# Performance work log

Hardware: AMD Instinct MI355X
Metric: run time of the kernel (lower is better)

Reference implementation:

```python
import jax, jax.numpy as jnp
import numpy as np

B, T, C, H = 4, 2048, 768, 12
D = C // H  # head dim = 64


def setup_inputs() -> dict:
    key = jax.random.key(0)
    ks = jax.random.split(key, 4)
    scale = 0.02
    return {
        "x": jax.random.normal(ks[0], (B, T, C), dtype=jnp.float32),
        "W_attn": jax.random.normal(ks[1], (C, 3 * C), dtype=jnp.float32) * scale,
        "b_attn": jnp.zeros((3 * C,), dtype=jnp.float32),
        "W_proj": jax.random.normal(ks[2], (C, C), dtype=jnp.float32) * scale,
        "b_proj": jnp.zeros((C,), dtype=jnp.float32),
    }


def reference(x, W_attn, b_attn, W_proj, b_proj):
    Bsz, Tlen, Cdim = x.shape
    qkv = x @ W_attn + b_attn                    # [B,T,3C]
    q, k, v = jnp.split(qkv, 3, axis=-1)          # each [B,T,C]
    # [B,T,C] -> [B,H,T,D]
    def heads(t):
        return t.reshape(Bsz, Tlen, H, D).transpose(0, 2, 1, 3)
    q, k, v = heads(q), heads(k), heads(v)
    att = jnp.einsum("bhqd,bhkd->bhqk", q, k) * (1.0 / np.sqrt(D))
    # causal mask: position q attends to k <= q
    mask = jnp.tril(jnp.ones((Tlen, Tlen), dtype=bool))
    att = jnp.where(mask[None, None], att, -jnp.inf)
    att = jax.nn.softmax(att, axis=-1)
    y = jnp.einsum("bhqk,bhkd->bhqd", att, v)     # [B,H,T,D]
    y = y.transpose(0, 2, 1, 3).reshape(Bsz, Tlen, Cdim)
    return y @ W_proj + b_proj
```

## Files before the change

kernel.cpp:

```cpp
#include <hip/hip_runtime.h>

#define B_SZ   4
#define T_LEN  2048
#define C_DIM  768
#define H_NUM  12
#define THREEC (3 * C_DIM)
#define M_ROWS (B_SZ * T_LEN)
#define CAST_N8 (M_ROWS * C_DIM / 8)
#define CAST_BLOCKS (CAST_N8 / 256)
#define TP_BX ((THREEC + C_DIM) / 32)
#define TP_BY (C_DIM / 32)

typedef _Float16 f16;
typedef _Float16 half8 __attribute__((ext_vector_type(8)));
typedef _Float16 half4 __attribute__((ext_vector_type(4)));
typedef __fp16   pk2   __attribute__((ext_vector_type(2)));
typedef float    f32x4 __attribute__((ext_vector_type(4)));

#define GLD16(gaddr, laddr)                                                         \
  __builtin_amdgcn_global_load_lds(                                                 \
      (const __attribute__((address_space(1))) unsigned int*)(gaddr),               \
      (__attribute__((address_space(3))) unsigned int*)(laddr), 16, 0, 0)
#define MFMA16(a, b, c) __builtin_amdgcn_mfma_f32_16x16x32_f16(a, b, c, 0, 0, 0)

__global__ __launch_bounds__(256) void prep_kernel(
    const float* __restrict__ x, f16* __restrict__ xh,
    const float* __restrict__ Wa, const float* __restrict__ Wp,
    f16* __restrict__ WtA, f16* __restrict__ WtP) {
  __shared__ f16 tile[32][33];
  const int bid = blockIdx.x;
  if (bid < CAST_BLOCKS) {
    int i = bid * 256 + threadIdx.x;
    const float* s = x + (size_t)i * 8;
    half8 h;
#pragma unroll
    for (int u = 0; u < 8; ++u) h[u] = (f16)s[u];
    *(half8*)(xh + (size_t)i * 8) = h;
    return;
  }
  const int t = bid - CAST_BLOCKS;
  int bx = t % TP_BX;
  const int by = t / TP_BX;
  const float* W; f16* Wt; int N;
  if (bx < THREEC / 32) { W = Wa; Wt = WtA; N = THREEC; }
  else { W = Wp; Wt = WtP; N = C_DIM; bx -= THREEC / 32; }
  const int n0 = bx * 32, k0 = by * 32;
  const int tx = threadIdx.x & 31, ty = threadIdx.x >> 5;
#pragma unroll
  for (int i = 0; i < 4; ++i)
    tile[ty + i * 8][tx] = (f16)W[(size_t)(k0 + ty + i * 8) * N + n0 + tx];
  __syncthreads();
#pragma unroll
  for (int i = 0; i < 4; ++i)
    Wt[(size_t)(n0 + ty + i * 8) * C_DIM + k0 + tx] = tile[tx][ty + i * 8];
}

template <int BM, int BN, int OUT_F16, int SWZ>
__global__ __launch_bounds__(256) void gemm_f16_kernel(
    const f16* __restrict__ A, const f16* __restrict__ Bt,
    const float* __restrict__ bias, f16* __restrict__ OutH,
    float* __restrict__ OutF, int M, int N, int K) {
  __shared__ f16 As[BM * 64];
  __shared__ f16 Bs[BN * 64];
  const int tid = threadIdx.x;
  const int lane = tid & 63, wave = tid >> 6;
  const int lm = lane & 15, kq = lane >> 4, lm7 = lm & 7;
  constexpr int MT = BM / 32, NT = BN / 32;
  const int wm = (wave & 1) * (BM / 2), wn = (wave >> 1) * (BN / 2);

  int bx = blockIdx.x, by = blockIdx.y;
  if (SWZ) {
    const int nx = gridDim.x;
    const int lin = by * nx + bx;
    const int cpx = (nx * gridDim.y) >> 3;
    const int swz = (lin & 7) * cpx + (lin >> 3);
    bx = swz % nx;
    by = swz / nx;
  }
  const int row0 = by * BM, col0 = bx * BN;

  f32x4 acc[MT][NT] = {};

  for (int k0 = 0; k0 < K; k0 += 64) {
    __syncthreads();
#pragma unroll
    for (int i = 0; i < BM / 32; ++i) {
      int c = tid + i * 256;
      int r = c >> 3, cc = (c & 7) ^ (r & 7);
      GLD16(&A[(size_t)(row0 + r) * K + k0 + cc * 8],
            &As[(i * 256 + wave * 64) * 8]);
    }
#pragma unroll
    for (int i = 0; i < BN / 32; ++i) {
      int c = tid + i * 256;
      int r = c >> 3, cc = (c & 7) ^ (r & 7);
      GLD16(&Bt[(size_t)(col0 + r) * K + k0 + cc * 8],
            &Bs[(i * 256 + wave * 64) * 8]);
    }
    __syncthreads();
#pragma unroll
    for (int ks = 0; ks < 2; ++ks) {
      const int pos = (ks * 4 + kq);
      half8 af[MT], bf[NT];
#pragma unroll
      for (int t = 0; t < MT; ++t)
        af[t] = *(const half8*)&As[(wm + t * 16 + lm) * 64 + (pos ^ lm7) * 8];
#pragma unroll
      for (int t = 0; t < NT; ++t)
        bf[t] = *(const half8*)&Bs[(wn + t * 16 + lm) * 64 + (pos ^ lm7) * 8];
#pragma unroll
      for (int mt = 0; mt < MT; ++mt)
#pragma unroll
        for (int nt = 0; nt < NT; ++nt)
          acc[mt][nt] = MFMA16(af[mt], bf[nt], acc[mt][nt]);
    }
  }

#pragma unroll
  for (int mt = 0; mt < MT; ++mt) {
    const int row = row0 + wm + mt * 16 + kq * 4;
#pragma unroll
    for (int nt = 0; nt < NT; ++nt) {
      const int col = col0 + wn + nt * 16 + lm;
      const float bv = bias[col];
#pragma unroll
      for (int r = 0; r < 4; ++r) {
        float v = acc[mt][nt][r] + bv;
        if (OUT_F16)
          OutH[(size_t)(row + r) * N + col] = (f16)v;
        else
          OutF[(size_t)(row + r) * N + col] = v;
      }
    }
  }
}

__global__ __launch_bounds__(256) void v_transpose_kernel(
    const f16* __restrict__ qkv, f16* __restrict__ vt) {
  __shared__ f16 tile[64 * 68];
  const int bh = blockIdx.x, b = bh / H_NUM, h = bh % H_NUM;
  const int t0 = blockIdx.y * 64;
  const int tid = threadIdx.x;
#pragma unroll
  for (int i = 0; i < 2; ++i) {
    int c = tid + i * 256;
    int tr = c >> 3, doff = (c & 7) * 8;
    int pcol = ((tr >> 5) << 5) | (((tr >> 2) & 3) << 3) |
               (((tr >> 4) & 1) << 2) | (tr & 3);
    half8 v = *(const half8*)&qkv[(size_t)(b * T_LEN + t0 + tr) * THREEC + 2 * C_DIM + h * 64 + doff];
#pragma unroll
    for (int u = 0; u < 8; ++u) tile[(doff + u) * 68 + pcol] = v[u];
  }
  __syncthreads();
#pragma unroll
  for (int i = 0; i < 2; ++i) {
    int c = tid + i * 256;
    int d = c >> 3, toff = (c & 7) * 8;
    half8 v;
#pragma unroll
    for (int u = 0; u < 8; ++u) v[u] = tile[d * 68 + toff + u];
    *(half8*)&vt[((size_t)bh * 64 + d) * T_LEN + t0 + toff] = v;
  }
}

__global__ __launch_bounds__(256, 3) void attn_kernel(
    const f16* __restrict__ qkv, const f16* __restrict__ vt,
    f16* __restrict__ y) {
  __shared__ f16 Kt[2][64 * 64];
  __shared__ f16 Vt[2][64 * 64];

  const int bh = blockIdx.x, b = bh / H_NUM, h = bh % H_NUM;
  const int yb = blockIdx.y;
  const int qb = 15 - yb;
  const int tid = threadIdx.x, lane = tid & 63, wave = tid >> 6;
  const int lm = lane & 15, kq = lane >> 4, lm7 = lm & 7;
  const int cw = qb * 2 + (wave >> 1);
  const int qw = qb * 128 + wave * 32;
  const f16 qscale = (f16)(0.125f * 1.44269504f);

  half8 vones;
#pragma unroll
  for (int u = 0; u < 8; ++u) vones[u] = (f16)1.f;

  half8 bq[2][2];
#pragma unroll
  for (int cq = 0; cq < 2; ++cq)
#pragma unroll
    for (int c2 = 0; c2 < 2; ++c2) {
      half8 v = *(const half8*)&qkv[(size_t)(b * T_LEN + qw + cq * 16 + lm) * THREEC +
                                    h * 64 + c2 * 32 + kq * 8];
      bq[cq][c2] = v * qscale;
    }

  f32x4 o[4][2] = {};
  f32x4 ol[2] = {};

  f32x4 fz = {};
  asm volatile("" : "+v"(fz));

  const int srow = tid >> 3;
  const int scol = ((tid & 7) ^ (srow & 7)) * 8;
  const f16* kp = &qkv[(size_t)(b * T_LEN + srow) * THREEC + C_DIM + h * 64 + scol];
  const f16* vp = &vt[((size_t)bh * 64 + srow) * T_LEN + scol];
  const size_t kp2 = (size_t)32 * THREEC;
  const size_t vp2 = (size_t)32 * T_LEN;

  const int sbase = wave * 512;

  const int n_tiles = qb * 2 + 2;

  GLD16(kp, &Kt[0][sbase]);
  GLD16(kp + kp2, &Kt[0][2048 + sbase]);
  GLD16(vp, &Vt[0][sbase]);
  GLD16(vp + vp2, &Vt[0][2048 + sbase]);
  kp += (size_t)64 * THREEC;
  vp += 64;

  for (int it = 0; it < n_tiles; ++it) {
    const int cur = it & 1;
    if (it + 1 < n_tiles) {
      GLD16(kp, &Kt[cur ^ 1][sbase]);
      GLD16(kp + kp2, &Kt[cur ^ 1][2048 + sbase]);
      GLD16(vp, &Vt[cur ^ 1][sbase]);
      GLD16(vp + vp2, &Vt[cur ^ 1][2048 + sbase]);
      kp += (size_t)64 * THREEC;
      vp += 64;
      asm volatile("s_waitcnt vmcnt(4)" ::: "memory");
    } else {
      asm volatile("s_waitcnt vmcnt(0)" ::: "memory");
    }
    __builtin_amdgcn_s_barrier();

    if (it <= cw) {
      f32x4 s4[4][2];
#pragma unroll
      for (int ct = 0; ct < 4; ++ct) {
        const f16* kr = &Kt[cur][(ct * 16 + lm) * 64];
        half8 ak0 = *(const half8*)&kr[(kq ^ lm7) * 8];
        half8 ak1 = *(const half8*)&kr[((4 + kq) ^ lm7) * 8];
#pragma unroll
        for (int cq = 0; cq < 2; ++cq) {
          f32x4 z = MFMA16(ak0, bq[cq][0], fz);
          s4[ct][cq] = MFMA16(ak1, bq[cq][1], z);
        }
      }
      if (it == cw) {
        const int j0 = it * 64;
#pragma unroll
        for (int ct = 0; ct < 4; ++ct)
#pragma unroll
          for (int cq = 0; cq < 2; ++cq) {
            const int qrow = qw + cq * 16 + lm;
#pragma unroll
            for (int r = 0; r < 4; ++r)
              if (j0 + ct * 16 + kq * 4 + r > qrow) s4[ct][cq][r] = -1e30f;
          }
      }
      union { half8 h8; pk2 p2[4]; } pa0[2], pa1[2];
#pragma unroll
      for (int cq = 0; cq < 2; ++cq) {
        pa0[cq].p2[0] = __builtin_amdgcn_cvt_pkrtz(
            __builtin_amdgcn_exp2f(s4[0][cq][0]), __builtin_amdgcn_exp2f(s4[0][cq][1]));
        pa0[cq].p2[1] = __builtin_amdgcn_cvt_pkrtz(
            __builtin_amdgcn_exp2f(s4[0][cq][2]), __builtin_amdgcn_exp2f(s4[0][cq][3]));
        pa0[cq].p2[2] = __builtin_amdgcn_cvt_pkrtz(
            __builtin_amdgcn_exp2f(s4[1][cq][0]), __builtin_amdgcn_exp2f(s4[1][cq][1]));
        pa0[cq].p2[3] = __builtin_amdgcn_cvt_pkrtz(
            __builtin_amdgcn_exp2f(s4[1][cq][2]), __builtin_amdgcn_exp2f(s4[1][cq][3]));
        pa1[cq].p2[0] = __builtin_amdgcn_cvt_pkrtz(
            __builtin_amdgcn_exp2f(s4[2][cq][0]), __builtin_amdgcn_exp2f(s4[2][cq][1]));
        pa1[cq].p2[1] = __builtin_amdgcn_cvt_pkrtz(
            __builtin_amdgcn_exp2f(s4[2][cq][2]), __builtin_amdgcn_exp2f(s4[2][cq][3]));
        pa1[cq].p2[2] = __builtin_amdgcn_cvt_pkrtz(
            __builtin_amdgcn_exp2f(s4[3][cq][0]), __builtin_amdgcn_exp2f(s4[3][cq][1]));
        pa1[cq].p2[3] = __builtin_amdgcn_cvt_pkrtz(
            __builtin_amdgcn_exp2f(s4[3][cq][2]), __builtin_amdgcn_exp2f(s4[3][cq][3]));
      }

#pragma unroll
      for (int dt = 0; dt < 4; ++dt) {
        const f16* vr = &Vt[cur][(dt * 16 + lm) * 64];
        half8 bv0 = *(const half8*)&vr[(kq ^ lm7) * 8];
        half8 bv1 = *(const half8*)&vr[((4 + kq) ^ lm7) * 8];
#pragma unroll
        for (int cq = 0; cq < 2; ++cq) {
          o[dt][cq] = MFMA16(pa0[cq].h8, bv0, o[dt][cq]);
          o[dt][cq] = MFMA16(pa1[cq].h8, bv1, o[dt][cq]);
        }
      }
#pragma unroll
      for (int cq = 0; cq < 2; ++cq) {
        ol[cq] = MFMA16(pa0[cq].h8, vones, ol[cq]);
        ol[cq] = MFMA16(pa1[cq].h8, vones, ol[cq]);
      }
    }

    __builtin_amdgcn_s_barrier();
  }

#pragma unroll
  for (int cq = 0; cq < 2; ++cq)
#pragma unroll
    for (int r = 0; r < 4; ++r) {
      const float inv = 1.f / ol[cq][r];
      const size_t base =
          (size_t)(b * T_LEN + qw + cq * 16 + kq * 4 + r) * C_DIM + h * 64;
#pragma unroll
      for (int dt = 0; dt < 4; ++dt)
        y[base + dt * 16 + lm] = (f16)(o[dt][cq][r] * inv);
    }
}

extern "C" void kernel_launch(void* const* d_in, const int* in_sizes, int n_in,
                              void* d_out, int out_size, void* d_ws, size_t ws_size,
                              hipStream_t stream) {
  const float* x      = (const float*)d_in[0];
  const float* W_attn = (const float*)d_in[1];
  const float* b_attn = (const float*)d_in[2];
  const float* W_proj = (const float*)d_in[3];
  const float* b_proj = (const float*)d_in[4];
  float* out = (float*)d_out;

  const int M = M_ROWS;
  auto align256 = [](size_t v) { return (v + 255) & ~(size_t)255; };
  char* ws = (char*)d_ws;
  f16* xh   = (f16*)ws; ws += align256((size_t)M * C_DIM * 2);
  f16* WtA  = (f16*)ws; ws += align256((size_t)THREEC * C_DIM * 2);
  f16* WtP  = (f16*)ws; ws += align256((size_t)C_DIM * C_DIM * 2);
  f16* qkvh = (f16*)ws; ws += align256((size_t)M * THREEC * 2);
  f16* vtg  = (f16*)ws; ws += align256((size_t)B_SZ * H_NUM * 64 * T_LEN * 2);
  f16* yh   = (f16*)ws; ws += align256((size_t)M * C_DIM * 2);

  prep_kernel<<<CAST_BLOCKS + TP_BX * TP_BY, 256, 0, stream>>>(
      x, xh, W_attn, W_proj, WtA, WtP);

  gemm_f16_kernel<128, 128, 1, 1><<<dim3(THREEC / 128, M / 128), 256, 0, stream>>>(
      xh, WtA, b_attn, qkvh, nullptr, M, THREEC, C_DIM);

  v_transpose_kernel<<<dim3(B_SZ * H_NUM, T_LEN / 64), 256, 0, stream>>>(qkvh, vtg);

  attn_kernel<<<dim3(B_SZ * H_NUM, 16), 256, 0, stream>>>(qkvh, vtg, yh);

  gemm_f16_kernel<128, 64, 0, 1><<<dim3(C_DIM / 64, M / 128), 256, 0, stream>>>(
      yh, WtP, b_proj, nullptr, out, M, C_DIM, C_DIM);
}
```

Measured before the change: 187.7 us.

## Double-buffer GEMM LDS tiles with K=32 stages and async prefetch

Replaces the single-buffered K=64 LDS tile loop in the f16 GEMM with a two-stage double buffer of K=32 tiles. The next tile is prefetched with global_load_lds while MFMAs run on the current one, using explicit vmcnt waits and raw s_barrier instead of __syncthreads. The XOR swizzle is adapted to 4 chunks per row. This is meant to hide global-load latency, at the cost of halving K work per barrier, adding a second barrier per iteration, and relying on hand-counted vmcnt values that must match the number of issued loads.

```diff
diff --git a/kernel.cpp b/kernel.cpp
--- a/kernel.cpp
+++ b/kernel.cpp
@@ -60,11 +60,13 @@
     const f16* __restrict__ A, const f16* __restrict__ Bt,
     const float* __restrict__ bias, f16* __restrict__ OutH,
     float* __restrict__ OutF, int M, int N, int K) {
-  __shared__ f16 As[BM * 64];
-  __shared__ f16 Bs[BN * 64];
+  __shared__ f16 As[2][BM * 32];
+  __shared__ f16 Bs[2][BN * 32];
   const int tid = threadIdx.x;
   const int lane = tid & 63, wave = tid >> 6;
-  const int lm = lane & 15, kq = lane >> 4, lm7 = lm & 7;
+  const int lm = lane & 15, kq = lane >> 4;
+  const int lmx = (lm >> 1) & 3;
+  const int rchunk = (kq ^ lmx) * 8;
   constexpr int MT = BM / 32, NT = BN / 32;
   const int wm = (wave & 1) * (BM / 2), wn = (wave >> 1) * (BN / 2);
 
@@ -81,39 +83,53 @@
 
   f32x4 acc[MT][NT] = {};
 
-  for (int k0 = 0; k0 < K; k0 += 64) {
-    __syncthreads();
-#pragma unroll
-    for (int i = 0; i < BM / 32; ++i) {
+  auto stage = [&](int kt, int buf) {
+    const int kof = kt * 32;
+#pragma unroll
+    for (int i = 0; i < BM / 64; ++i) {
       int c = tid + i * 256;
-      int r = c >> 3, cc = (c & 7) ^ (r & 7);
-      GLD16(&A[(size_t)(row0 + r) * K + k0 + cc * 8],
-            &As[(i * 256 + wave * 64) * 8]);
-    }
-#pragma unroll
-    for (int i = 0; i < BN / 32; ++i) {
+      int r = c >> 2, cc = (c & 3) ^ ((r >> 1) & 3);
+      GLD16(&A[(size_t)(row0 + r) * K + kof + cc * 8],
+            &As[buf][(i * 256 + wave * 64) * 8]);
+    }
+#pragma unroll
+    for (int i = 0; i < BN / 64; ++i) {
       int c = tid + i * 256;
-      int r = c >> 3, cc = (c & 7) ^ (r & 7);
-      GLD16(&Bt[(size_t)(col0 + r) * K + k0 + cc * 8],
-            &Bs[(i * 256 + wave * 64) * 8]);
-    }
-    __syncthreads();
-#pragma unroll
-    for (int ks = 0; ks < 2; ++ks) {
-      const int pos = (ks * 4 + kq);
-      half8 af[MT], bf[NT];
-#pragma unroll
-      for (int t = 0; t < MT; ++t)
-        af[t] = *(const half8*)&As[(wm + t * 16 + lm) * 64 + (pos ^ lm7) * 8];
-#pragma unroll
-      for (int t = 0; t < NT; ++t)
-        bf[t] = *(const half8*)&Bs[(wn + t * 16 + lm) * 64 + (pos ^ lm7) * 8];
-#pragma unroll
-      for (int mt = 0; mt < MT; ++mt)
-#pragma unroll
-        for (int nt = 0; nt < NT; ++nt)
-          acc[mt][nt] = MFMA16(af[mt], bf[nt], acc[mt][nt]);
-    }
+      int r = c >> 2, cc = (c & 3) ^ ((r >> 1) & 3);
+      GLD16(&Bt[(size_t)(col0 + r) * K + kof + cc * 8],
+            &Bs[buf][(i * 256 + wave * 64) * 8]);
+    }
+  };
+
+  const int nk = K >> 5;
+  stage(0, 0);
+  for (int kt = 0; kt < nk; ++kt) {
+    const int cur = kt & 1;
+    if (kt + 1 < nk) {
+      stage(kt + 1, cur ^ 1);
+      if constexpr ((BM + BN) / 64 == 4)
+        asm volatile("s_waitcnt vmcnt(4)" ::: "memory");
+      else
+        asm volatile("s_waitcnt vmcnt(3)" ::: "memory");
+    } else {
+      asm volatile("s_waitcnt vmcnt(0)" ::: "memory");
+    }
+    __builtin_amdgcn_s_barrier();
+
+    half8 af[MT], bf[NT];
+#pragma unroll
+    for (int t = 0; t < MT; ++t)
+      af[t] = *(const half8*)&As[cur][(wm + t * 16 + lm) * 32 + rchunk];
+#pragma unroll
+    for (int t = 0; t < NT; ++t)
+      bf[t] = *(const half8*)&Bs[cur][(wn + t * 16 + lm) * 32 + rchunk];
+#pragma unroll
+    for (int mt = 0; mt < MT; ++mt)
+#pragma unroll
+      for (int nt = 0; nt < NT; ++nt)
+        acc[mt][nt] = MFMA16(af[mt], bf[nt], acc[mt][nt]);
+
+    __builtin_amdgcn_s_barrier();
   }
 
 #pragma unroll
```

New measurement: 192.8 us. 2.7% more time.
